# Kernel optimization log

Hardware: AMD Instinct MI355X
Metric: run time of the kernel (lower is better)

The kernel has to match this reference:

```python
import jax, jax.numpy as jnp
import numpy as np
jax.config.update("jax_enable_x64", True)

WINDOW_SHAPE = (16, 16, 8)
SPARSE_SHAPE = (512, 512, 64)
GROUP_SIZE = 128
BATCH_COUNTS = np.array([500000, 480123, 510007, 495870], dtype=np.int64)  # not multiples of 128 -> padding path active


def setup_inputs() -> dict:
    key = jax.random.key(0)
    kx, ky, kz = jax.random.split(key, 3)
    N = int(BATCH_COUNTS.sum())
    bids = jnp.asarray(np.repeat(np.arange(len(BATCH_COUNTS), dtype=np.int64), BATCH_COUNTS))
    x = jax.random.randint(kx, (N,), 0, SPARSE_SHAPE[0], dtype=jnp.int64)
    y = jax.random.randint(ky, (N,), 0, SPARSE_SHAPE[1], dtype=jnp.int64)
    z = jax.random.randint(kz, (N,), 0, SPARSE_SHAPE[2], dtype=jnp.int64)
    coords = jnp.stack([bids, x, y, z], axis=1)  # [N,4] int64: (batch, x, y, z)
    return {"coords": coords, "batch_size": 4}


def _hash_keys(coords, shifted):
    n, m, l = SPARSE_SHAPE
    n2o, m2o, l2o = WINDOW_SHAPE
    n1 = int(np.ceil(n / n2o) + 1)
    m1 = int(np.ceil(m / m2o) + 1)
    l1 = int(np.ceil(l / l2o) + 1)
    if shifted:
        x = coords[:, 1] + n2o // 2
        y = coords[:, 2] + m2o // 2
        z = coords[:, 3] + l2o // 2
    else:
        x, y, z = coords[:, 1], coords[:, 2], coords[:, 3]
    x1, y1, z1 = x // n2o, y // m2o, z // l2o
    x2, y2, z2 = x % n2o, y % m2o, z % l2o
    # original code triples both window and grid-of-window extents before hashing
    n2, m2, l2 = 3 * n2o, 3 * m2o, 3 * l2o
    n1, m1, l1 = 3 * n1, 3 * m1, 3 * l1
    sx = 1 - 2 * (x1 & 1)  # (-1)**x1
    sy = 1 - 2 * (y1 & 1)
    sz = 1 - 2 * (z1 & 1)
    s2x = 1 - 2 * (x2 & 1)
    s2y = 1 - 2 * (y2 & 1)
    s2z = 1 - 2 * (z2 & 1)
    boff = coords[:, 0] * (n * m * l * 10)
    vx = (n1 * y1 + n1 * m1 * z1 + sy * x1) * (n2 * m2 * l2) + sy * (m2 * x2 + n2 * m2 * z2 + s2x * y2) + boff
    vy = (m1 * z1 + m1 * l1 * x1 + sz * y1) * (m2 * l2 * n2) + sz * (l2 * y2 + m2 * l2 * x2 + s2y * z2) + boff
    vz = (l1 * x1 + l1 * n1 * y1 + sx * z1) * (l2 * n2 * m2) + sx * (n2 * z2 + l2 * n2 * y2 + s2z * x2) + boff
    return vx, vy, vz


def reference(coords, batch_size):
    G = GROUP_SIZE
    coords = coords.astype(jnp.int64)
    bids = coords[:, 0]
    N = coords.shape[0]
    num_per_batch = jax.ops.segment_sum(jnp.ones((N,), jnp.int64), bids, num_segments=batch_size)
    bs = jnp.concatenate([jnp.zeros((1,), jnp.int64), jnp.cumsum(num_per_batch)])
    num_per_batch_p = ((num_per_batch + G - 1) // G) * G
    bsp = jnp.concatenate([jnp.zeros((1,), jnp.int64), jnp.cumsum(num_per_batch_p)])
    Np = int(bsp[-1])  # concrete (not under jit); padded total length

    # win2flat[j] = j + (bsp[b] - bs[b]) for b = batch of element j (coords assumed batch-sorted)
    win2flat = jnp.arange(N, dtype=jnp.int64) + (bsp[:-1] - bs[:-1])[bids]

    # flat2win: identity within each padded batch, with the padded tail replicated
    # from one group earlier, then shifted back to flat indexing.
    p = jnp.arange(Np, dtype=jnp.int64)
    b = jnp.searchsorted(bsp, p, side="right") - 1  # batch of each padded slot
    r = num_per_batch % G
    pad_tail = (r[b] != 0) & (p >= bsp[b + 1] - G + r[b])
    flat2win = p - G * pad_tail.astype(jnp.int64) - (bsp[b] - bs[b])

    outs = [flat2win, win2flat]
    for shifted in (False, True):
        vx, vy, vz = _hash_keys(coords, shifted)
        outs.append(jnp.argsort(vx))
        outs.append(jnp.argsort(vy))
        outs.append(jnp.argsort(vz))
    # (flat2win, win2flat, x, y, z, x_shift, y_shift, z_shift)
    return tuple(outs)
```

## Files before the change

### kernel.cpp

```cpp
#include <hip/hip_runtime.h>
#include <type_traits>

typedef unsigned long long u64;
typedef unsigned int u32;

#define BLOCK     256
#define WAVES     4
#define TILE      4096
#define SUBT      1024
#define CHUNKS    16
#define KSHIFT    21
#define KBIAS     (1LL << 21)
#define KMASK     ((1u << 21) - 1)
#define GRP       128


__device__ __forceinline__ void hash3(long long x, long long y, long long z,
                                      long long boff, long long* v) {
  long long x1 = x >> 4, y1 = y >> 4, z1 = z >> 3;
  long long x2 = x & 15, y2 = y & 15, z2 = z & 7;
  long long sx  = 1 - 2*(x1 & 1), sy  = 1 - 2*(y1 & 1), sz  = 1 - 2*(z1 & 1);
  long long s2x = 1 - 2*(x2 & 1), s2y = 1 - 2*(y2 & 1), s2z = 1 - 2*(z2 & 1);
  v[0] = (99*y1 + 9801*z1 + sy*x1)*55296 + sy*(48*x2 + 2304*z2 + s2x*y2) + boff;
  v[1] = (99*z1 + 2673*x1 + sz*y1)*55296 + sz*(24*y2 + 1152*x2 + s2y*z2) + boff;
  v[2] = (27*x1 + 2673*y1 + sx*z1)*55296 + sx*(48*z2 + 1152*y2 + s2z*x2) + boff;
}

__global__ void count_k(const int* __restrict__ coords, unsigned* __restrict__ counts, int N) {
  __shared__ unsigned c[8];
  if (threadIdx.x < 8) c[threadIdx.x] = 0;
  __syncthreads();
  for (int i = blockIdx.x*blockDim.x + threadIdx.x; i < N; i += gridDim.x*blockDim.x)
    atomicAdd(&c[coords[4*i] & 7], 1u);
  __syncthreads();
  if (threadIdx.x < 8) atomicAdd(&counts[threadIdx.x], c[threadIdx.x]);
}

__global__ void prefix_k(const unsigned* __restrict__ counts, long long* __restrict__ meta,
                         const int* __restrict__ bsz) {
  int NB = *bsz; if (NB > 8) NB = 8;
  long long run_bs = 0, run_bsp = 0;
  meta[0] = 0;
  for (int b = 0; b < NB; b++) {
    long long c  = (long long)counts[b];
    long long cp = (c + GRP - 1) / GRP * GRP;
    long long r  = c % GRP;
    meta[9 + b]  = run_bsp - run_bs;
    meta[17 + b] = r ? (run_bsp + cp - GRP + r) : 0x7fffffffffffffffLL;
    run_bs += c; run_bsp += cp;
    meta[b + 1] = run_bsp;
  }
  meta[25] = run_bsp;
  meta[26] = NB;
}

__global__ void flat2win_k(const long long* __restrict__ meta, int* __restrict__ dout) {
  long long p = (long long)blockIdx.x * blockDim.x + threadIdx.x;
  long long Np = meta[25];
  if (p >= Np) return;
  int NB = (int)meta[26];
  int b = 0;
  while (b < NB - 1 && meta[b + 1] <= p) b++;
  long long pad = (p >= meta[17 + b]) ? 1 : 0;
  dout[p] = (int)(p - GRP * pad - meta[9 + b]);
}

__global__ void __launch_bounds__(BLOCK) keygen_k(const int* __restrict__ coords,
                                                  u64* __restrict__ keys,
                                                  u32* __restrict__ hist,
                                                  const long long* __restrict__ meta,
                                                  int* __restrict__ dout,
                                                  int N, int B, int g0, int g, int doAux) {
  __shared__ u32 cnt[6 * 256];
  int b = blockIdx.x, tid = threadIdx.x;
  int nb = g * 256;
  for (int j = tid; j < nb; j += BLOCK) cnt[j] = 0;
  __syncthreads();
  long long Np = meta[25];
  for (int t = 0; t < CHUNKS; t++) {
    int i = b * TILE + t * BLOCK + tid;
    if (i < N) {
      int4 c4 = ((const int4*)coords)[i];
      long long boff = (long long)c4.x * 167772160LL;
      long long v[6];
      hash3(c4.y,     c4.z,     c4.w,     boff, v);
      hash3(c4.y + 8, c4.z + 8, c4.w + 4, boff, v + 3);
      #pragma unroll
      for (int s = 0; s < 6; s++) {
        if (s >= g0 && s < g0 + g) {
          u64 kb = (u64)(v[s] + KBIAS);
          keys[(size_t)(s - g0) * N + i] = (kb << KSHIFT) | (unsigned)i;
          atomicAdd(&cnt[(s - g0) * 256 + ((unsigned)kb & 255)], 1u);
        }
      }
      if (doAux) dout[Np + i] = (int)(i + meta[9 + c4.x]);
    }
  }
  __syncthreads();
  for (int j = tid; j < nb; j += BLOCK) {
    int s = j >> 8, d = j & 255;
    hist[((size_t)s * B + b) * 256 + d] = cnt[j];
  }
}

template<typename KT, int RADIXN, int SHIFT>
__global__ void __launch_bounds__(BLOCK) hist_k(const KT* __restrict__ src,
                                                u32* __restrict__ hist, int N, int B) {
  __shared__ u32 cnt[RADIXN];
  int s = blockIdx.y, b = blockIdx.x, tid = threadIdx.x;
  for (int j = tid; j < RADIXN; j += BLOCK) cnt[j] = 0;
  __syncthreads();
  const KT* in = src + (size_t)s * N;
  #pragma unroll 4
  for (int t = 0; t < CHUNKS; t++) {
    int i = b * TILE + t * BLOCK + tid;
    if (i < N) {
      unsigned d = (unsigned)(in[i] >> SHIFT) & (RADIXN - 1);
      atomicAdd(&cnt[d], 1u);
    }
  }
  __syncthreads();
  for (int j = tid; j < RADIXN; j += BLOCK) hist[((size_t)s * B + b) * RADIXN + j] = cnt[j];
}

template<int RADIXN>
__global__ void __launch_bounds__(BLOCK) scan_k(u32* __restrict__ hist,
                                                u32* __restrict__ dbase, int B) {
  __shared__ u32 tot[RADIXN];
  int s = blockIdx.x, tid = threadIdx.x;
  for (int d = tid; d < RADIXN; d += BLOCK) {
    u32 run = 0; int b = 0;
    for (; b + 8 <= B; b += 8) {
      u32 v[8];
      #pragma unroll
      for (int j = 0; j < 8; j++) v[j] = hist[((size_t)s * B + b + j) * RADIXN + d];
      #pragma unroll
      for (int j = 0; j < 8; j++) { hist[((size_t)s * B + b + j) * RADIXN + d] = run; run += v[j]; }
    }
    for (; b < B; b++) {
      size_t x = ((size_t)s * B + b) * RADIXN + d;
      u32 v = hist[x]; hist[x] = run; run += v;
    }
    tot[d] = run;
  }
  __syncthreads();
  if (tid < 64) {
    u32 run = 0;
    #pragma unroll
    for (int c = 0; c < (RADIXN + 63) / 64; c++) {
      int dd = c * 64 + tid;
      u32 v = (dd < RADIXN) ? tot[dd] : 0, x = v;
      for (int off = 1; off < 64; off <<= 1) { u32 u = __shfl_up(x, off); if (tid >= off) x += u; }
      if (dd < RADIXN) dbase[(size_t)s * 512 + dd] = run + x - v;
      run += __shfl(x, 63);
    }
  }
}

template<int RB, int SHIFT, int MODE>
__global__ void __launch_bounds__(BLOCK) scatter_k(const void* __restrict__ srcv,
                                                   void* __restrict__ dstv,
                                                   const u32* __restrict__ hist,
                                                   const u32* __restrict__ dbase,
                                                   int N, int B,
                                                   int* __restrict__ dout,
                                                   const long long* __restrict__ meta, int g0) {
  constexpr int RADIXN = 1 << RB;
  constexpr int DPT = (RADIXN + BLOCK - 1) / BLOCK;
  using KT = typename std::conditional<MODE == 2, u32, u64>::type;
  using ST = typename std::conditional<MODE == 0, u64, u32>::type;
  __shared__ ST items[TILE];
  __shared__ unsigned short dig[MODE == 1 ? TILE : 64];
  __shared__ unsigned short cnt[WAVES][RADIXN];
  __shared__ int exf[RADIXN];
  int s = blockIdx.y, b = blockIdx.x, tid = threadIdx.x;
  int wave = tid >> 6, lane = tid & 63;
  for (int j = tid; j < WAVES * RADIXN; j += BLOCK) ((unsigned short*)cnt)[j] = 0;
  __syncthreads();

  const KT* in = (const KT*)srcv + (size_t)s * N;
  int subbase = b * TILE + wave * SUBT;
  bool full = (subbase + SUBT <= N);
  KT k[CHUNKS]; u32 pd[CHUNKS];
  if (full) {
    #pragma unroll
    for (int t = 0; t < CHUNKS; t++) k[t] = in[subbase + t * 64 + lane];
    #pragma unroll
    for (int t = 0; t < CHUNKS; t++) {
      unsigned d = (unsigned)(k[t] >> SHIFT) & (RADIXN - 1);
      u64 m = ~0ull;
      #pragma unroll
      for (int bit = 0; bit < RB; bit++) {
        u64 bal = __ballot((d >> bit) & 1);
        m &= ((d >> bit) & 1) ? bal : ~bal;
      }
      unsigned rank = __builtin_amdgcn_mbcnt_hi((u32)(m >> 32),
                        __builtin_amdgcn_mbcnt_lo((u32)m, 0u));
      unsigned pbase = cnt[wave][d];
      pd[t] = d | ((pbase + rank) << RB);
      if (rank == 0) cnt[wave][d] = (unsigned short)(pbase + (unsigned)__popcll(m));
    }
  } else {
    #pragma unroll
    for (int t = 0; t < CHUNKS; t++) k[t] = in[min(subbase + t * 64 + lane, N - 1)];
    #pragma unroll
    for (int t = 0; t < CHUNKS; t++) {
      int i = subbase + t * 64 + lane;
      bool valid = i < N;
      unsigned d = (unsigned)(k[t] >> SHIFT) & (RADIXN - 1);
      u64 m = __ballot(valid);
      #pragma unroll
      for (int bit = 0; bit < RB; bit++) {
        u64 bal = __ballot(valid && ((d >> bit) & 1));
        m &= ((d >> bit) & 1) ? bal : ~bal;
      }
      unsigned rank = __builtin_amdgcn_mbcnt_hi((u32)(m >> 32),
                        __builtin_amdgcn_mbcnt_lo((u32)m, 0u));
      unsigned pbase = cnt[wave][d];
      pd[t] = d | ((pbase + rank) << RB);
      if (valid && rank == 0) cnt[wave][d] = (unsigned short)(pbase + (unsigned)__popcll(m));
    }
  }
  __syncthreads();

  u32 sc[DPT][3];
  #pragma unroll
  for (int q = 0; q < DPT; q++) {
    int d = q * BLOCK + tid;
    u32 a0 = cnt[0][d], a1 = cnt[1][d], a2 = cnt[2][d], a3 = cnt[3][d];
    sc[q][0] = a0; sc[q][1] = a1; sc[q][2] = a2;
    exf[d] = (int)(a0 + a1 + a2 + a3);
  }
  __syncthreads();
  if (tid < 64) {
    u32 run = 0;
    #pragma unroll
    for (int c = 0; c < (RADIXN + 63) / 64; c++) {
      int dd = c * 64 + tid;
      u32 v = (u32)exf[dd], x = v;
      for (int off = 1; off < 64; off <<= 1) { u32 u = __shfl_up(x, off); if (tid >= off) x += u; }
      exf[dd] = (int)(run + x - v);
      run += __shfl(x, 63);
    }
  }
  __syncthreads();
  const u32* hrow = hist + (size_t)(s * B + b) * RADIXN;
  const u32* brow = dbase + (size_t)s * 512;
  #pragma unroll
  for (int q = 0; q < DPT; q++) {
    int d = q * BLOCK + tid;
    int e = exf[d];
    u32 gb = hrow[d] + brow[d];
    cnt[0][d] = (unsigned short)e;
    cnt[1][d] = (unsigned short)(e + sc[q][0]);
    cnt[2][d] = (unsigned short)(e + sc[q][0] + sc[q][1]);
    cnt[3][d] = (unsigned short)(e + sc[q][0] + sc[q][1] + sc[q][2]);
    exf[d] = (int)gb - e;
  }
  __syncthreads();

  #pragma unroll
  for (int t = 0; t < CHUNKS; t++) {
    int i = subbase + t * 64 + lane;
    if (i < N) {
      unsigned d = pd[t] & (RADIXN - 1);
      unsigned lr = pd[t] >> RB;
      unsigned pos = (unsigned)cnt[wave][d] + lr;
      if constexpr (MODE == 1) {
        items[pos] = (u32)(((k[t] >> 46) << 21) | ((u32)k[t] & KMASK));
        dig[pos] = (unsigned short)d;
      } else {
        items[pos] = (ST)k[t];
      }
    }
  }
  __syncthreads();

  int validCount = N - b * TILE; if (validCount > TILE) validCount = TILE;
  long long obase = 0;
  if (MODE == 2) obase = meta[25] + (long long)N * (1 + g0 + s);
  u64* out64 = (u64*)dstv + (size_t)s * N;
  u32* out32 = (u32*)dstv + (size_t)s * N;
  #pragma unroll 4
  for (int t = 0; t < CHUNKS; t++) {
    int j = t * BLOCK + tid;
    if (j < validCount) {
      ST kk = items[j];
      if constexpr (MODE == 0) {
        unsigned d = (unsigned)(kk >> SHIFT) & (RADIXN - 1);
        out64[exf[d] + j] = kk;
      } else if constexpr (MODE == 1) {
        unsigned d = dig[j];
        out32[exf[d] + j] = kk;
      } else {
        unsigned d = (unsigned)(kk >> SHIFT) & (RADIXN - 1);
        dout[obase + exf[d] + j] = (int)(kk & KMASK);
      }
    }
  }
}

extern "C" void kernel_launch(void* const* d_in, const int* in_sizes, int n_in,
                              void* d_out, int out_size, void* d_ws, size_t ws_size,
                              hipStream_t stream) {
  const int* coords = (const int*)d_in[0];
  const int* bsz    = (const int*)d_in[1];
  int N = in_sizes[0] / 4;
  int* dout = (int*)d_out;
  char* ws = (char*)d_ws;
  int B = (N + TILE - 1) / TILE;

  auto align256 = [](size_t x) { return (x + 255) & ~(size_t)255; };

  int g = 1;
  size_t offHist = 512, offBase = 0, offA = 0, offB = 0;
  const int cands[4] = {6, 3, 2, 1};
  for (int ci = 0; ci < 4; ci++) {
    int cg = cands[ci];
    size_t oBs = offHist + (size_t)cg * B * 512 * 4;
    size_t oA = align256(oBs + (size_t)cg * 512 * 4);
    size_t oB = oA + (size_t)cg * N * 8;
    size_t need = oB + (size_t)cg * N * 8;
    if (need <= ws_size || cg == 1) {
      g = cg; offBase = oBs; offA = oA; offB = oB;
      if (need <= ws_size) break;
    }
  }

  unsigned*  counts = (unsigned*)ws;
  long long* meta   = (long long*)(ws + 64);
  u32*       hist   = (u32*)(ws + offHist);
  u32*       dbase  = (u32*)(ws + offBase);
  u64*       keysA  = (u64*)(ws + offA);
  u64*       keysB  = (u64*)(ws + offB);

  hipMemsetAsync(ws, 0, 512, stream);
  count_k<<<1024, 256, 0, stream>>>(coords, counts, N);
  prefix_k<<<1, 1, 0, stream>>>(counts, meta, bsz);
  flat2win_k<<<(N + 8 * GRP + 255) / 256, 256, 0, stream>>>(meta, dout);

  for (int g0 = 0; g0 < 6; g0 += g) {
    keygen_k<<<B, BLOCK, 0, stream>>>(coords, keysA, hist, meta, dout, N, B, g0, g, g0 == 0);
    scan_k<256><<<g, BLOCK, 0, stream>>>(hist, dbase, B);
    scatter_k<8, 21, 0><<<dim3(B, g), BLOCK, 0, stream>>>(keysA, keysB, hist, dbase, N, B,
                                                          dout, meta, g0);
    hist_k<u64, 256, 29><<<dim3(B, g), BLOCK, 0, stream>>>(keysB, hist, N, B);
    scan_k<256><<<g, BLOCK, 0, stream>>>(hist, dbase, B);
    scatter_k<8, 29, 0><<<dim3(B, g), BLOCK, 0, stream>>>(keysB, keysA, hist, dbase, N, B,
                                                          dout, meta, g0);
    hist_k<u64, 512, 37><<<dim3(B, g), BLOCK, 0, stream>>>(keysA, hist, N, B);
    scan_k<512><<<g, BLOCK, 0, stream>>>(hist, dbase, B);
    scatter_k<9, 37, 1><<<dim3(B, g), BLOCK, 0, stream>>>(keysA, keysB, hist, dbase, N, B,
                                                          dout, meta, g0);
    hist_k<u32, 256, 21><<<dim3(B, g), BLOCK, 0, stream>>>((const u32*)keysB, hist, N, B);
    scan_k<256><<<g, BLOCK, 0, stream>>>(hist, dbase, B);
    scatter_k<8, 21, 2><<<dim3(B, g), BLOCK, 0, stream>>>(keysB, keysA, hist, dbase, N, B,
                                                          dout, meta, g0);
  }
}
```

Measured before the change: 474.4 us.

## Transpose radix histogram to digit-major and split scan into parallel two-stage kernels

Histograms are now stored digit-major (digit, block) instead of block-major. This lets a new scanA kernel give each wave one digit row and scan it with coalesced loads and wave shuffles across many workgroups. The old kernel ran only g workgroups, with a serial per-thread loop over blocks. A small scanB kernel then computes the exclusive prefix over digit totals. The scatter kernel also remaps its block index so that consecutive work lands on the same XCD, at the cost of an extra launch per pass and strided histogram writes.

```diff
diff --git a/kernel.cpp b/kernel.cpp
--- a/kernel.cpp
+++ b/kernel.cpp
@@ -99,7 +99,7 @@
   __syncthreads();
   for (int j = tid; j < nb; j += BLOCK) {
     int s = j >> 8, d = j & 255;
-    hist[((size_t)s * B + b) * 256 + d] = cnt[j];
+    hist[((size_t)s * 256 + d) * B + b] = cnt[j];
   }
 }
 
@@ -120,40 +120,40 @@
     }
   }
   __syncthreads();
-  for (int j = tid; j < RADIXN; j += BLOCK) hist[((size_t)s * B + b) * RADIXN + j] = cnt[j];
+  for (int j = tid; j < RADIXN; j += BLOCK) hist[((size_t)s * RADIXN + j) * B + b] = cnt[j];
 }
 
 template<int RADIXN>
-__global__ void __launch_bounds__(BLOCK) scan_k(u32* __restrict__ hist,
-                                                u32* __restrict__ dbase, int B) {
-  __shared__ u32 tot[RADIXN];
+__global__ void __launch_bounds__(BLOCK) scanA_k(u32* __restrict__ hist,
+                                                 u32* __restrict__ dbase, int B) {
+  int s = blockIdx.y;
+  int d = blockIdx.x * WAVES + (threadIdx.x >> 6);
+  int lane = threadIdx.x & 63;
+  u32* row = hist + ((size_t)s * RADIXN + d) * B;
+  u32 run = 0;
+  for (int b0 = 0; b0 < B; b0 += 64) {
+    int b = b0 + lane;
+    u32 v = (b < B) ? row[b] : 0;
+    u32 x = v;
+    #pragma unroll
+    for (int off = 1; off < 64; off <<= 1) { u32 u = __shfl_up(x, off); if (lane >= off) x += u; }
+    if (b < B) row[b] = run + x - v;
+    run += __shfl(x, 63);
+  }
+  if (lane == 0) dbase[(size_t)s * 512 + d] = run;
+}
+
+template<int RADIXN>
+__global__ void __launch_bounds__(64) scanB_k(u32* __restrict__ dbase) {
   int s = blockIdx.x, tid = threadIdx.x;
-  for (int d = tid; d < RADIXN; d += BLOCK) {
-    u32 run = 0; int b = 0;
-    for (; b + 8 <= B; b += 8) {
-      u32 v[8];
-      #pragma unroll
-      for (int j = 0; j < 8; j++) v[j] = hist[((size_t)s * B + b + j) * RADIXN + d];
-      #pragma unroll
-      for (int j = 0; j < 8; j++) { hist[((size_t)s * B + b + j) * RADIXN + d] = run; run += v[j]; }
-    }
-    for (; b < B; b++) {
-      size_t x = ((size_t)s * B + b) * RADIXN + d;
-      u32 v = hist[x]; hist[x] = run; run += v;
-    }
-    tot[d] = run;
-  }
-  __syncthreads();
-  if (tid < 64) {
-    u32 run = 0;
-    #pragma unroll
-    for (int c = 0; c < (RADIXN + 63) / 64; c++) {
-      int dd = c * 64 + tid;
-      u32 v = (dd < RADIXN) ? tot[dd] : 0, x = v;
-      for (int off = 1; off < 64; off <<= 1) { u32 u = __shfl_up(x, off); if (tid >= off) x += u; }
-      if (dd < RADIXN) dbase[(size_t)s * 512 + dd] = run + x - v;
-      run += __shfl(x, 63);
-    }
+  u32 run = 0;
+  #pragma unroll
+  for (int c = 0; c < RADIXN / 64; c++) {
+    int dd = c * 64 + tid;
+    u32 v = dbase[(size_t)s * 512 + dd], x = v;
+    for (int off = 1; off < 64; off <<= 1) { u32 u = __shfl_up(x, off); if (tid >= off) x += u; }
+    dbase[(size_t)s * 512 + dd] = run + x - v;
+    run += __shfl(x, 63);
   }
 }
 
@@ -173,7 +173,16 @@
   __shared__ unsigned short dig[MODE == 1 ? TILE : 64];
   __shared__ unsigned short cnt[WAVES][RADIXN];
   __shared__ int exf[RADIXN];
-  int s = blockIdx.y, b = blockIdx.x, tid = threadIdx.x;
+  int s, b;
+  {
+    int nwg = B * (int)gridDim.y;
+    int lin = (int)blockIdx.y * B + (int)blockIdx.x;
+    int qc = nwg >> 3, rc = nwg & 7;
+    int xcd = lin & 7, pos = lin >> 3;
+    int swz = (xcd < rc ? xcd * (qc + 1) : rc * (qc + 1) + (xcd - rc) * qc) + pos;
+    s = swz / B; b = swz - s * B;
+  }
+  int tid = threadIdx.x;
   int wave = tid >> 6, lane = tid & 63;
   for (int j = tid; j < WAVES * RADIXN; j += BLOCK) ((unsigned short*)cnt)[j] = 0;
   __syncthreads();
@@ -244,13 +253,12 @@
     }
   }
   __syncthreads();
-  const u32* hrow = hist + (size_t)(s * B + b) * RADIXN;
   const u32* brow = dbase + (size_t)s * 512;
   #pragma unroll
   for (int q = 0; q < DPT; q++) {
     int d = q * BLOCK + tid;
     int e = exf[d];
-    u32 gb = hrow[d] + brow[d];
+    u32 gb = hist[((size_t)s * RADIXN + d) * B + b] + brow[d];
     cnt[0][d] = (unsigned short)e;
     cnt[1][d] = (unsigned short)(e + sc[q][0]);
     cnt[2][d] = (unsigned short)(e + sc[q][0] + sc[q][1]);
@@ -341,19 +349,23 @@
 
   for (int g0 = 0; g0 < 6; g0 += g) {
     keygen_k<<<B, BLOCK, 0, stream>>>(coords, keysA, hist, meta, dout, N, B, g0, g, g0 == 0);
-    scan_k<256><<<g, BLOCK, 0, stream>>>(hist, dbase, B);
+    scanA_k<256><<<dim3(256 / WAVES, g), BLOCK, 0, stream>>>(hist, dbase, B);
+    scanB_k<256><<<g, 64, 0, stream>>>(dbase);
     scatter_k<8, 21, 0><<<dim3(B, g), BLOCK, 0, stream>>>(keysA, keysB, hist, dbase, N, B,
                                                           dout, meta, g0);
     hist_k<u64, 256, 29><<<dim3(B, g), BLOCK, 0, stream>>>(keysB, hist, N, B);
-    scan_k<256><<<g, BLOCK, 0, stream>>>(hist, dbase, B);
+    scanA_k<256><<<dim3(256 / WAVES, g), BLOCK, 0, stream>>>(hist, dbase, B);
+    scanB_k<256><<<g, 64, 0, stream>>>(dbase);
     scatter_k<8, 29, 0><<<dim3(B, g), BLOCK, 0, stream>>>(keysB, keysA, hist, dbase, N, B,
                                                           dout, meta, g0);
     hist_k<u64, 512, 37><<<dim3(B, g), BLOCK, 0, stream>>>(keysA, hist, N, B);
-    scan_k<512><<<g, BLOCK, 0, stream>>>(hist, dbase, B);
+    scanA_k<512><<<dim3(512 / WAVES, g), BLOCK, 0, stream>>>(hist, dbase, B);
+    scanB_k<512><<<g, 64, 0, stream>>>(dbase);
     scatter_k<9, 37, 1><<<dim3(B, g), BLOCK, 0, stream>>>(keysA, keysB, hist, dbase, N, B,
                                                           dout, meta, g0);
     hist_k<u32, 256, 21><<<dim3(B, g), BLOCK, 0, stream>>>((const u32*)keysB, hist, N, B);
-    scan_k<256><<<g, BLOCK, 0, stream>>>(hist, dbase, B);
+    scanA_k<256><<<dim3(256 / WAVES, g), BLOCK, 0, stream>>>(hist, dbase, B);
+    scanB_k<256><<<g, 64, 0, stream>>>(dbase);
     scatter_k<8, 21, 2><<<dim3(B, g), BLOCK, 0, stream>>>(keysB, keysA, hist, dbase, N, B,
                                                           dout, meta, g0);
   }
```

Result: faster. 394.6 us (-16.8%).
